# Kernel tuning notes

Hardware: AMD Instinct MI355X
Metric: run time of the kernel (lower is better)

## Reference

```python
import jax, jax.numpy as jnp
import numpy as np

SELECTOR = jnp.array([29, 49, 79])
N_FINAL = 6
N_EM_ITERS = 10
LOG_2PI = float(np.log(2.0 * np.pi))


def _logdet2(c):
    # log determinant of trailing 2x2 matrices
    return jnp.log(c[..., 0, 0] * c[..., 1, 1] - c[..., 0, 1] * c[..., 1, 0])


def _inv2(c):
    # analytic inverse of trailing 2x2 matrices
    det = c[..., 0, 0] * c[..., 1, 1] - c[..., 0, 1] * c[..., 1, 0]
    inv = jnp.stack([
        jnp.stack([c[..., 1, 1], -c[..., 0, 1]], axis=-1),
        jnp.stack([-c[..., 1, 0], c[..., 0, 0]], axis=-1),
    ], axis=-2)
    return inv / det[..., None, None]


def _initial_state(probas, trajectories):
    B, M = probas.shape
    tsel = trajectories[:, :, SELECTOR, :]                       # [B,M,3,2]
    dots = jnp.einsum('bmtd,bntd->btmn', tsel, tsel)             # [B,3,M,M]
    d1 = jnp.einsum('bmtd,bmtd->btm', tsel, tsel)                # [B,3,M]
    R = jnp.sqrt(d1[:, :, :, None] + d1[:, :, None, :] - 2.0 * dots)
    thr = jnp.quantile(R[:, -1].reshape(B, -1), 0.15, axis=-1)[:, None, None, None]
    adj = (R <= thr).astype(probas.dtype).prod(axis=1)           # [B,M,M]
    worked = jnp.ones((B, M), dtype=probas.dtype)
    bidx = jnp.arange(B)
    idxs = []
    for _ in range(N_FINAL):
        score = (adj * probas[:, None, :]).sum(axis=2) * worked  # [B,M]
        amax = jnp.argmax(score, axis=-1)                        # [B]
        worked = worked * (1.0 - adj[bidx, amax])
        idxs.append(amax)
    return jnp.stack(idxs, axis=1)                               # [B,6]


def _coefficients(cov6, trajectories, traj6, probas6):
    cov6_sel = cov6[:, :, SELECTOR]                              # [B,6,3,2,2]
    prec = _inv2(cov6_sel)                                       # [B,6,3,2,2]
    diff = traj6[:, :, SELECTOR][:, :, None] - trajectories[:, :, SELECTOR][:, None]  # [B,6,M,3,2]
    qform = jnp.einsum('bnmti,bntij,bnmtj->bnmt', diff, prec, diff)
    logdet = _logdet2(cov6_sel)[:, :, None, :]                   # [B,6,1,3]
    pM = jnp.exp((-LOG_2PI - 0.5 * logdet - 0.5 * qform).sum(axis=-1)) + 1e-8  # [B,6,M]
    num = pM * probas6[:, :, None]
    return num / (num.sum(axis=1, keepdims=True) + 1e-8)


def _forward(non_normalized_probas, trajectories, covariance_matrices):
    B = trajectories.shape[0]
    probas = jax.nn.softmax(non_normalized_probas, axis=-1)
    idx = jax.lax.stop_gradient(_initial_state(probas, trajectories))  # [B,6]
    b = jnp.arange(B)[:, None]
    traj6 = trajectories[b, idx]                                 # [B,6,T,2]
    probas6 = jax.nn.softmax(jnp.take_along_axis(non_normalized_probas, idx, axis=1), axis=-1)
    cov6 = covariance_matrices[b, idx]                           # [B,6,T,2,2]
    for _ in range(N_EM_ITERS):
        pM = jax.lax.stop_gradient(_coefficients(cov6, trajectories, traj6, probas6))
        P = probas[:, None, :] * pM                              # [B,6,M]
        probas6 = P.sum(axis=-1)                                 # [B,6]
        traj6 = jnp.einsum('bnm,bmtd->bntd', P, trajectories) / probas6[:, :, None, None]
        diff = traj6[:, :, None] - trajectories[:, None]         # [B,6,M,T,2]
        cov6 = (jnp.einsum('bnm,bmtij->bntij', P, covariance_matrices)
                + jnp.einsum('bnm,bnmti,bnmtj->bntij', P, diff, diff)) / probas6[:, :, None, None, None]
    return probas6, traj6, cov6


def setup_inputs() -> dict:
    key = jax.random.key(0)
    k1, k2, k3 = jax.random.split(key, 3)
    B, M, T = 256, 48, 80
    logits = jax.random.normal(k1, (B, M), dtype=jnp.float32)
    trajectories = jax.random.normal(k2, (B, M, T, 2), dtype=jnp.float32)
    A = 0.3 * jax.random.normal(k3, (B, M, T, 2, 2), dtype=jnp.float32)
    cov = A @ jnp.swapaxes(A, -1, -2) + 0.5 * jnp.eye(2, dtype=jnp.float32)
    return {'non_normalized_probas': logits, 'trajectories': trajectories,
            'covariance_matrices': cov}


def reference(non_normalized_probas, trajectories, covariance_matrices):
    return _forward(non_normalized_probas, trajectories, covariance_matrices)
```

## Files before the change

### kernel.cpp

```cpp
#include <hip/hip_runtime.h>
#include <math.h>

#define BATCH 256
#define M 48
#define T 80
#define NF 6
#define EMIT 10
#define MM (M*M)
#define NPT (MM/256)

#define LOG2PI 1.8378770664093453f

__global__ __launch_bounds__(256, 1)
void em_kernel(const float* __restrict__ g_logits,
               const float* __restrict__ g_traj,
               const float* __restrict__ g_cov,
               float* __restrict__ g_out)
{
    const int b = blockIdx.x;
    const int tid = threadIdx.x;
    const int lane = tid & 63;
    const int wv = tid >> 6;
    const int SEL[3] = {29, 49, 79};

    __shared__ __align__(16) float s_fxy[M*T*2];
    __shared__ __align__(16) float s_fc01[M*T*2];
    __shared__ float s_fc11[M*T];
    __shared__ float s_R2[MM];
    __shared__ float s_logits[M];
    __shared__ float s_probas[M];
    __shared__ float s_tsel[M*6];
    __shared__ float s_d1[M*3];
    __shared__ __align__(16) float s_csel[M*3*4];
    __shared__ __align__(16) float s_Pm[M*8];
    __shared__ float s_t6sel[NF*6];
    __shared__ float s_probas6[NF];
    __shared__ float s_prec[NF*3*3];
    __shared__ float s_ld[NF*3];
    __shared__ int   s_idx[NF];
    __shared__ unsigned s_hist[256];
    __shared__ unsigned s_wsum[4];
    __shared__ int s_seld;
    __shared__ int s_sele;

    const float* traj_b = g_traj + (size_t)b * (M*T*2);
    const float* cov_b  = g_cov  + (size_t)b * (M*T*4);

    if (tid < M) s_logits[tid] = g_logits[b*M + tid];
    {
        const float4* src = (const float4*)traj_b;
        float4* dst = (float4*)s_fxy;
        for (int i = tid; i < (M*T*2)/4; i += 256) dst[i] = src[i];
    }
    {
        const float4* src = (const float4*)cov_b;
        float2* dstc = (float2*)s_fc01;
        for (int i = tid; i < M*T; i += 256) {
            float4 c = src[i];
            dstc[i] = make_float2(c.x, c.y);
            s_fc11[i] = c.w;
        }
    }
    __syncthreads();

    if (wv == 0) {
        float lg = (lane < M) ? s_logits[lane] : -1e30f;
        float mx = lg;
        #pragma unroll
        for (int off = 32; off; off >>= 1) mx = fmaxf(mx, __shfl_xor(mx, off));
        float e = (lane < M) ? expf(lg - mx) : 0.f;
        float sum = e;
        #pragma unroll
        for (int off = 32; off; off >>= 1) sum += __shfl_xor(sum, off);
        if (lane < M) s_probas[lane] = e / sum;
    }
    if (tid >= 64 && tid < 64 + M*3) {
        int i = tid - 64;
        int m = i / 3, tt = i - (i/3)*3;
        float x = s_fxy[(m*T + SEL[tt])*2 + 0];
        float y = s_fxy[(m*T + SEL[tt])*2 + 1];
        s_tsel[m*6+tt*2+0] = x;
        s_tsel[m*6+tt*2+1] = y;
        s_d1[i] = x*x + y*y;
    }
    if (tid < M*3) {
        int m = tid / 3, tt = tid - (tid/3)*3;
        int src = m*T + SEL[tt];
        s_csel[tid*4+0] = s_fc01[src*2+0];
        s_csel[tid*4+1] = s_fc01[src*2+1];
        s_csel[tid*4+2] = s_fc11[src];
        s_csel[tid*4+3] = 0.f;
    }
    __syncthreads();

    for (int e = tid; e < MM; e += 256) {
        int m = e / M, n = e - (e/M)*M;
        float dot = s_tsel[m*6+4]*s_tsel[n*6+4] + s_tsel[m*6+5]*s_tsel[n*6+5];
        float v = s_d1[m*3+2] + s_d1[n*3+2] - 2.0f*dot;
        s_R2[e] = sqrtf(fmaxf(v, 0.0f));
    }
    __syncthreads();

    unsigned key[NPT];
    #pragma unroll
    for (int c = 0; c < NPT; ++c) key[c] = __float_as_uint(s_R2[tid + c*256]);

    int target = 345;
    unsigned prefix = 0u, pmask = 0u;
    for (int shift = 24; shift >= 0; shift -= 8) {
        s_hist[tid] = 0u;
        __syncthreads();
        #pragma unroll
        for (int c = 0; c < NPT; ++c) {
            if ((key[c] & pmask) == prefix)
                atomicAdd(&s_hist[(key[c] >> shift) & 255u], 1u);
        }
        __syncthreads();
        unsigned h = s_hist[tid];
        unsigned v = h;
        #pragma unroll
        for (int off = 1; off < 64; off <<= 1) {
            unsigned u = __shfl_up(v, off);
            if (lane >= off) v += u;
        }
        if (lane == 63) s_wsum[wv] = v;
        __syncthreads();
        unsigned pre = 0;
        for (int w = 0; w < wv; ++w) pre += s_wsum[w];
        unsigned exc = pre + v - h;
        if ((int)exc <= target && target < (int)(exc + h)) {
            s_seld = tid;
            s_sele = (int)exc;
        }
        __syncthreads();
        target -= s_sele;
        prefix |= ((unsigned)s_seld) << shift;
        pmask  |= (255u << shift);
    }
    const unsigned k1 = prefix;
    const float v1f = __uint_as_float(k1);

    {
        unsigned cnt = 0, mng = 0xFFFFFFFFu;
        #pragma unroll
        for (int c = 0; c < NPT; ++c) {
            if (key[c] <= k1) cnt++;
            else mng = (key[c] < mng) ? key[c] : mng;
        }
        #pragma unroll
        for (int off = 32; off > 0; off >>= 1) {
            cnt += __shfl_down(cnt, off);
            unsigned mo = __shfl_down(mng, off);
            mng = (mo < mng) ? mo : mng;
        }
        if (lane == 0) { s_hist[wv] = cnt; s_hist[4+wv] = mng; }
        __syncthreads();
        unsigned ctot = s_hist[0]+s_hist[1]+s_hist[2]+s_hist[3];
        unsigned mtot = s_hist[4];
        if (s_hist[5] < mtot) mtot = s_hist[5];
        if (s_hist[6] < mtot) mtot = s_hist[6];
        if (s_hist[7] < mtot) mtot = s_hist[7];
        unsigned k2 = (ctot >= 347u) ? k1 : mtot;
        const float v2f = __uint_as_float(k2);
        const float qi = 0.15f * 2303.0f;
        const float fr = qi - floorf(qi);
        float thr = v1f * (1.0f - fr) + v2f * fr;

        for (int e = tid; e < MM; e += 256) {
            int m = e / M, n = e - (e/M)*M;
            bool a = (s_R2[e] <= thr);
            float d0 = s_tsel[m*6+0]*s_tsel[n*6+0] + s_tsel[m*6+1]*s_tsel[n*6+1];
            float r0 = sqrtf(fmaxf(s_d1[m*3+0] + s_d1[n*3+0] - 2.0f*d0, 0.0f));
            float d1v = s_tsel[m*6+2]*s_tsel[n*6+2] + s_tsel[m*6+3]*s_tsel[n*6+3];
            float r1 = sqrtf(fmaxf(s_d1[m*3+1] + s_d1[n*3+1] - 2.0f*d1v, 0.0f));
            a = a && (r0 <= thr) && (r1 <= thr);
            s_R2[e] = a ? 1.0f : 0.0f;
        }
    }
    __syncthreads();
    #define s_adj s_R2

    if (wv == 0) {
        const int m = (lane < M) ? lane : (M-1);
        float adjcol[M];
        #pragma unroll
        for (int n = 0; n < M; ++n) adjcol[n] = s_adj[n*M + m];
        float base = 0.f;
        #pragma unroll
        for (int n = 0; n < M; ++n) base += adjcol[n] * s_probas[n];
        float worked = 1.f;
        #pragma unroll
        for (int k = 0; k < NF; ++k) {
            float sc = (lane < M) ? base * worked : -1.f;
            int bi = lane;
            #pragma unroll
            for (int off = 32; off; off >>= 1) {
                float so = __shfl_down(sc, off);
                int io = __shfl_down(bi, off);
                if (so > sc || (so == sc && io < bi)) { sc = so; bi = io; }
            }
            int amax = __shfl(bi, 0);
            if (lane == 0) s_idx[k] = amax;
            float arow = s_adj[amax*M + m];
            worked *= (1.f - arow);
        }
        if (lane < NF) {
            float mx = -1e30f;
            for (int j = 0; j < NF; ++j) mx = fmaxf(mx, s_logits[s_idx[j]]);
            float sum = 0.f;
            for (int j = 0; j < NF; ++j) sum += expf(s_logits[s_idx[j]] - mx);
            s_probas6[lane] = expf(s_logits[s_idx[lane]] - mx) / sum;
        }
        if (lane < NF*3) {
            int n = lane / 3, tt = lane - (lane/3)*3;
            int m0 = s_idx[n];
            s_t6sel[n*6+tt*2+0] = s_tsel[m0*6+tt*2+0];
            s_t6sel[n*6+tt*2+1] = s_tsel[m0*6+tt*2+1];
            float c00 = s_csel[(m0*3+tt)*4+0];
            float c01 = s_csel[(m0*3+tt)*4+1];
            float c11 = s_csel[(m0*3+tt)*4+2];
            float det = c00*c11 - c01*c01;
            s_prec[lane*3+0] =  c11 / det;
            s_prec[lane*3+1] = -c01 / det;
            s_prec[lane*3+2] =  c00 / det;
            s_ld[lane] = logf(det);
        }
    }
    __syncthreads();

    for (int it = 0; it < EMIT; ++it) {
        if (wv == 0) {
            const int m = (lane < M) ? lane : (M-1);
            float tm[6];
            #pragma unroll
            for (int j = 0; j < 6; ++j) tm[j] = s_tsel[m*6+j];
            float num[NF];
            float den = 1e-8f;
            #pragma unroll
            for (int n = 0; n < NF; ++n) {
                float q = 0.f, lds_ = 0.f;
                #pragma unroll
                for (int tt = 0; tt < 3; ++tt) {
                    float dx = s_t6sel[n*6+tt*2+0] - tm[tt*2+0];
                    float dy = s_t6sel[n*6+tt*2+1] - tm[tt*2+1];
                    float p00 = s_prec[(n*3+tt)*3+0];
                    float p01 = s_prec[(n*3+tt)*3+1];
                    float p11 = s_prec[(n*3+tt)*3+2];
                    q += p00*dx*dx + 2.0f*p01*dx*dy + p11*dy*dy;
                    lds_ += s_ld[n*3+tt];
                }
                float ex = -3.0f*LOG2PI - 0.5f*lds_ - 0.5f*q;
                num[n] = (expf(ex) + 1e-8f) * s_probas6[n];
                den += num[n];
            }
            float f = (lane < M) ? (s_probas[m] / den) : 0.f;
            float P[NF];
            #pragma unroll
            for (int n = 0; n < NF; ++n) P[n] = (lane < M) ? num[n]*f : 0.f;
            float s[NF];
            #pragma unroll
            for (int n = 0; n < NF; ++n) {
                float v = P[n];
                #pragma unroll
                for (int off = 32; off; off >>= 1) v += __shfl_down(v, off);
                s[n] = v;
            }
            if (lane < M) {
                *(float4*)&s_Pm[m*8]   = make_float4(P[0],P[1],P[2],P[3]);
                *(float2*)&s_Pm[m*8+4] = make_float2(P[4],P[5]);
            }
            if (lane == 0) {
                #pragma unroll
                for (int n = 0; n < NF; ++n) s_probas6[n] = s[n];
            }
        }
        __syncthreads();

        if (it < EMIT-1) {
            if (wv == 0 && lane < NF*3) {
                int n = lane / 3, tt = lane - (lane/3)*3;
                float S1x=0,S1y=0,Sxx=0,Sxy=0,Syy=0,C00=0,C01=0,C11=0;
                for (int m2 = 0; m2 < M; ++m2) {
                    float x = s_tsel[m2*6+tt*2+0];
                    float y = s_tsel[m2*6+tt*2+1];
                    float4 c = *(const float4*)&s_csel[(m2*3+tt)*4];
                    float p = s_Pm[m2*8+n];
                    S1x += p*x; S1y += p*y;
                    Sxx += p*x*x; Sxy += p*x*y; Syy += p*y*y;
                    C00 += p*c.x; C01 += p*c.y; C11 += p*c.z;
                }
                float p6 = s_probas6[n];
                float tx = S1x/p6, ty = S1y/p6;
                float c00 = (C00 + (Sxx - S1x*tx)) / p6;
                float c01 = (C01 + (Sxy - S1x*ty)) / p6;
                float c11 = (C11 + (Syy - S1y*ty)) / p6;
                float det = c00*c11 - c01*c01;
                s_prec[lane*3+0] =  c11 / det;
                s_prec[lane*3+1] = -c01 / det;
                s_prec[lane*3+2] =  c00 / det;
                s_ld[lane] = logf(det);
                s_t6sel[n*6+tt*2+0] = tx;
                s_t6sel[n*6+tt*2+1] = ty;
            }
            __syncthreads();
        }
    }

    float* out_p = g_out;
    float2* out_t = (float2*)(g_out + BATCH*NF);
    float4* out_c = (float4*)(g_out + BATCH*NF + BATCH*NF*T*2);
    if (tid < 240) {
        int np = tid / 80;
        int t  = tid - np*80;
        int n0 = np*2, n1 = n0 + 1;
        float S1x0=0,S1y0=0,Sxx0=0,Sxy0=0,Syy0=0,C000=0,C010=0,C110=0;
        float S1x1=0,S1y1=0,Sxx1=0,Sxy1=0,Syy1=0,C001=0,C011=0,C111=0;
        const float2* fxy = (const float2*)s_fxy;
        const float2* fc01 = (const float2*)s_fc01;
        const float2* pm2 = (const float2*)s_Pm;
        #pragma unroll 8
        for (int m2 = 0; m2 < M; ++m2) {
            float2 xy  = fxy[m2*T + t];
            float2 c01 = fc01[m2*T + t];
            float  c11 = s_fc11[m2*T + t];
            float2 pp  = pm2[m2*4 + np];
            float xx = xy.x*xy.x, xyv = xy.x*xy.y, yy = xy.y*xy.y;
            S1x0 += pp.x*xy.x;  S1y0 += pp.x*xy.y;
            Sxx0 += pp.x*xx;    Sxy0 += pp.x*xyv;  Syy0 += pp.x*yy;
            C000 += pp.x*c01.x; C010 += pp.x*c01.y; C110 += pp.x*c11;
            S1x1 += pp.y*xy.x;  S1y1 += pp.y*xy.y;
            Sxx1 += pp.y*xx;    Sxy1 += pp.y*xyv;  Syy1 += pp.y*yy;
            C001 += pp.y*c01.x; C011 += pp.y*c01.y; C111 += pp.y*c11;
        }
        float p60 = s_probas6[n0], p61 = s_probas6[n1];
        float tx0 = S1x0/p60, ty0 = S1y0/p60;
        float tx1 = S1x1/p61, ty1 = S1y1/p61;
        float c000 = (C000 + (Sxx0 - S1x0*tx0)) / p60;
        float c010 = (C010 + (Sxy0 - S1x0*ty0)) / p60;
        float c110 = (C110 + (Syy0 - S1y0*ty0)) / p60;
        float c001 = (C001 + (Sxx1 - S1x1*tx1)) / p61;
        float c011 = (C011 + (Sxy1 - S1x1*ty1)) / p61;
        float c111 = (C111 + (Syy1 - S1y1*ty1)) / p61;
        size_t base = (size_t)b*(NF*T);
        out_t[base + n0*T + t] = make_float2(tx0, ty0);
        out_t[base + n1*T + t] = make_float2(tx1, ty1);
        out_c[base + n0*T + t] = make_float4(c000, c010, c010, c110);
        out_c[base + n1*T + t] = make_float4(c001, c011, c011, c111);
    }
    if (tid < NF) out_p[b*NF + tid] = s_probas6[tid];
}

extern "C" void kernel_launch(void* const* d_in, const int* in_sizes, int n_in,
                              void* d_out, int out_size, void* d_ws, size_t ws_size,
                              hipStream_t stream) {
    const float* logits = (const float*)d_in[0];
    const float* traj   = (const float*)d_in[1];
    const float* cov    = (const float*)d_in[2];
    float* out = (float*)d_out;
    em_kernel<<<dim3(BATCH), dim3(256), 0, stream>>>(logits, traj, cov, out);
}
```

Before: 122.3 us.

## Rewrite EM kernel as single-wavefront block with async LDS loads and histogram quantile

Shrinks each block from 256 threads to one 64-lane wavefront, which removes all __syncthreads barriers. Bulk trajectory and covariance data are copied with global_load_lds DMA, split into stages so the copies overlap the distance, quantile and greedy-selection work. The 4-pass radix select becomes a value-scaled histogram plus a candidate rank within the chosen bin. The EM M-step is spread across 54 lanes, and the final per-timestep reduction now runs 64 lanes over all six components. Risks include less parallelism per block for the final reduction, correctness of the bin-candidate cap of 192, and reliance on a raw s_waitcnt value plus the DMA writes being visible to LDS reads.

```diff
diff --git a/kernel.cpp b/kernel.cpp
--- a/kernel.cpp
+++ b/kernel.cpp
@@ -7,26 +7,27 @@
 #define NF 6
 #define EMIT 10
 #define MM (M*M)
-#define NPT (MM/256)
-
+#define KPL (MM/64)
+#define NBIN 256
+#define CAP 192
 #define LOG2PI 1.8378770664093453f
 
-__global__ __launch_bounds__(256, 1)
+typedef unsigned int u32;
+typedef unsigned long long u64;
+
+__global__ __launch_bounds__(64, 1)
 void em_kernel(const float* __restrict__ g_logits,
                const float* __restrict__ g_traj,
                const float* __restrict__ g_cov,
                float* __restrict__ g_out)
 {
     const int b = blockIdx.x;
-    const int tid = threadIdx.x;
-    const int lane = tid & 63;
-    const int wv = tid >> 6;
+    const int lane = threadIdx.x;
     const int SEL[3] = {29, 49, 79};
 
-    __shared__ __align__(16) float s_fxy[M*T*2];
-    __shared__ __align__(16) float s_fc01[M*T*2];
-    __shared__ float s_fc11[M*T];
-    __shared__ float s_R2[MM];
+    __shared__ __align__(16) float s_txy[M*T*2];
+    __shared__ __align__(16) float s_cv4[M*T*4];
+    __shared__ float s_adj[MM];
     __shared__ float s_logits[M];
     __shared__ float s_probas[M];
     __shared__ float s_tsel[M*6];
@@ -38,160 +39,182 @@
     __shared__ float s_prec[NF*3*3];
     __shared__ float s_ld[NF*3];
     __shared__ int   s_idx[NF];
-    __shared__ unsigned s_hist[256];
-    __shared__ unsigned s_wsum[4];
-    __shared__ int s_seld;
-    __shared__ int s_sele;
-
-    const float* traj_b = g_traj + (size_t)b * (M*T*2);
-    const float* cov_b  = g_cov  + (size_t)b * (M*T*4);
-
-    if (tid < M) s_logits[tid] = g_logits[b*M + tid];
+    __shared__ u32   s_hist[NBIN];
+    __shared__ u32   s_cand[CAP];
+    __shared__ u32   s_cnt;
+    __shared__ float s_v[2];
+
+    const float* traj_b = g_traj + (size_t)b*(M*T*2);
+    const float* cov_b  = g_cov  + (size_t)b*(M*T*4);
+
+    float myLogit = -1e30f;
+    if (lane < M) myLogit = g_logits[b*M + lane];
+    float selx[3], sely[3], cc0[3], cc1[3], cc2[3];
+    #pragma unroll
+    for (int r = 0; r < 3; ++r) {
+        int i = lane + r*64;
+        if (i < M*3) {
+            int m = i/3, tt = i - (i/3)*3;
+            float2 xy = ((const float2*)traj_b)[m*T + SEL[tt]];
+            float4 cv = ((const float4*)cov_b)[m*T + SEL[tt]];
+            selx[r]=xy.x; sely[r]=xy.y; cc0[r]=cv.x; cc1[r]=cv.y; cc2[r]=cv.w;
+        }
+    }
+    if (lane < M) s_logits[lane] = myLogit;
+    #pragma unroll
+    for (int r = 0; r < 3; ++r) {
+        int i = lane + r*64;
+        if (i < M*3) {
+            int m = i/3, tt = i - (i/3)*3;
+            s_tsel[m*6+tt*2+0] = selx[r];
+            s_tsel[m*6+tt*2+1] = sely[r];
+            s_d1[i] = selx[r]*selx[r] + sely[r]*sely[r];
+            s_csel[i*4+0]=cc0[r]; s_csel[i*4+1]=cc1[r]; s_csel[i*4+2]=cc2[r]; s_csel[i*4+3]=0.f;
+        }
+    }
+
+    __builtin_amdgcn_sched_barrier(0);
     {
-        const float4* src = (const float4*)traj_b;
-        float4* dst = (float4*)s_fxy;
-        for (int i = tid; i < (M*T*2)/4; i += 256) dst[i] = src[i];
-    }
-    {
-        const float4* src = (const float4*)cov_b;
-        float2* dstc = (float2*)s_fc01;
-        for (int i = tid; i < M*T; i += 256) {
-            float4 c = src[i];
-            dstc[i] = make_float2(c.x, c.y);
-            s_fc11[i] = c.w;
-        }
-    }
-    __syncthreads();
-
-    if (wv == 0) {
-        float lg = (lane < M) ? s_logits[lane] : -1e30f;
-        float mx = lg;
-        #pragma unroll
-        for (int off = 32; off; off >>= 1) mx = fmaxf(mx, __shfl_xor(mx, off));
-        float e = (lane < M) ? expf(lg - mx) : 0.f;
-        float sum = e;
-        #pragma unroll
-        for (int off = 32; off; off >>= 1) sum += __shfl_xor(sum, off);
-        if (lane < M) s_probas[lane] = e / sum;
-    }
-    if (tid >= 64 && tid < 64 + M*3) {
-        int i = tid - 64;
-        int m = i / 3, tt = i - (i/3)*3;
-        float x = s_fxy[(m*T + SEL[tt])*2 + 0];
-        float y = s_fxy[(m*T + SEL[tt])*2 + 1];
-        s_tsel[m*6+tt*2+0] = x;
-        s_tsel[m*6+tt*2+1] = y;
-        s_d1[i] = x*x + y*y;
-    }
-    if (tid < M*3) {
-        int m = tid / 3, tt = tid - (tid/3)*3;
-        int src = m*T + SEL[tt];
-        s_csel[tid*4+0] = s_fc01[src*2+0];
-        s_csel[tid*4+1] = s_fc01[src*2+1];
-        s_csel[tid*4+2] = s_fc11[src];
-        s_csel[tid*4+3] = 0.f;
-    }
-    __syncthreads();
-
-    for (int e = tid; e < MM; e += 256) {
-        int m = e / M, n = e - (e/M)*M;
+        const char* gt = (const char*)traj_b + lane*16;
+        #pragma unroll
+        for (int k = 0; k < 30; ++k)
+            __builtin_amdgcn_global_load_lds(
+                (const __attribute__((address_space(1))) u32*)(gt + k*1024),
+                (__attribute__((address_space(3))) u32*)((char*)s_txy + k*1024), 16, 0, 0);
+    }
+    __builtin_amdgcn_sched_barrier(0);
+
+    float mx = myLogit;
+    #pragma unroll
+    for (int off = 32; off; off >>= 1) mx = fmaxf(mx, __shfl_xor(mx, off));
+    float pe = (lane < M) ? expf(myLogit - mx) : 0.f;
+    float psum = pe;
+    #pragma unroll
+    for (int off = 32; off; off >>= 1) psum += __shfl_xor(psum, off);
+    const float proba = pe / psum;
+    if (lane < M) s_probas[lane] = proba;
+
+    float key[KPL];
+    #pragma unroll
+    for (int c = 0; c < KPL; ++c) {
+        int e = lane + c*64;
+        int m = e/M, n = e - (e/M)*M;
         float dot = s_tsel[m*6+4]*s_tsel[n*6+4] + s_tsel[m*6+5]*s_tsel[n*6+5];
         float v = s_d1[m*3+2] + s_d1[n*3+2] - 2.0f*dot;
-        s_R2[e] = sqrtf(fmaxf(v, 0.0f));
-    }
-    __syncthreads();
-
-    unsigned key[NPT];
-    #pragma unroll
-    for (int c = 0; c < NPT; ++c) key[c] = __float_as_uint(s_R2[tid + c*256]);
-
-    int target = 345;
-    unsigned prefix = 0u, pmask = 0u;
-    for (int shift = 24; shift >= 0; shift -= 8) {
-        s_hist[tid] = 0u;
-        __syncthreads();
-        #pragma unroll
-        for (int c = 0; c < NPT; ++c) {
-            if ((key[c] & pmask) == prefix)
-                atomicAdd(&s_hist[(key[c] >> shift) & 255u], 1u);
-        }
-        __syncthreads();
-        unsigned h = s_hist[tid];
-        unsigned v = h;
-        #pragma unroll
-        for (int off = 1; off < 64; off <<= 1) {
-            unsigned u = __shfl_up(v, off);
-            if (lane >= off) v += u;
-        }
-        if (lane == 63) s_wsum[wv] = v;
-        __syncthreads();
-        unsigned pre = 0;
-        for (int w = 0; w < wv; ++w) pre += s_wsum[w];
-        unsigned exc = pre + v - h;
-        if ((int)exc <= target && target < (int)(exc + h)) {
-            s_seld = tid;
-            s_sele = (int)exc;
-        }
-        __syncthreads();
-        target -= s_sele;
-        prefix |= ((unsigned)s_seld) << shift;
-        pmask  |= (255u << shift);
-    }
-    const unsigned k1 = prefix;
-    const float v1f = __uint_as_float(k1);
-
+        key[c] = sqrtf(fmaxf(v, 0.0f));
+    }
+    float kmax = 0.f;
+    #pragma unroll
+    for (int c = 0; c < KPL; ++c) kmax = fmaxf(kmax, key[c]);
+    #pragma unroll
+    for (int off = 32; off; off >>= 1) kmax = fmaxf(kmax, __shfl_xor(kmax, off));
+    const float scale = 256.0f / kmax;
+
+    s_hist[lane]=0; s_hist[lane+64]=0; s_hist[lane+128]=0; s_hist[lane+192]=0;
+    #pragma unroll
+    for (int c = 0; c < KPL; ++c) {
+        int bin = (int)(key[c]*scale); bin = bin > 255 ? 255 : bin;
+        atomicAdd(&s_hist[bin], 1u);
+    }
+    uint4 hv = ((const uint4*)s_hist)[lane];
+    u32 s4 = hv.x + hv.y + hv.z + hv.w;
+    u32 cum = s4;
+    #pragma unroll
+    for (int off = 1; off < 64; off <<= 1) {
+        u32 u = __shfl_up(cum, off);
+        if (lane >= off) cum += u;
+    }
+
+    #pragma unroll 1
+    for (int ri = 0; ri < 2; ++ri) {
+        const u32 target = 345u + (u32)ri;
+        u64 bmask = __ballot(cum > target);
+        int g = __builtin_ctzll(bmask);
+        int binIdx = 0; u32 binStart = 0;
+        if (lane == g) {
+            u32 exc = cum - s4;
+            int bi2 = lane*4;
+            if (exc + hv.x > target)      { binIdx = bi2;   binStart = exc; }
+            else { exc += hv.x;
+                if (exc + hv.y > target)  { binIdx = bi2+1; binStart = exc; }
+                else { exc += hv.y;
+                    if (exc + hv.z > target) { binIdx = bi2+2; binStart = exc; }
+                    else { exc += hv.z;       binIdx = bi2+3; binStart = exc; } } }
+        }
+        binIdx   = __shfl(binIdx, g);
+        binStart = (u32)__shfl((int)binStart, g);
+        if (lane == 0) s_cnt = 0;
+        #pragma unroll
+        for (int c = 0; c < KPL; ++c) {
+            int bin = (int)(key[c]*scale); bin = bin > 255 ? 255 : bin;
+            if (bin == binIdx) {
+                u32 p = atomicAdd(&s_cnt, 1u);
+                if (p < CAP) s_cand[p] = __float_as_uint(key[c]);
+            }
+        }
+        u32 cnt = s_cnt; if (cnt > CAP) cnt = CAP;
+        u32 own0=0xFFFFFFFFu, own1=0xFFFFFFFFu, own2=0xFFFFFFFFu;
+        if ((u32)lane      < cnt) own0 = s_cand[lane];
+        if ((u32)lane+64u  < cnt) own1 = s_cand[lane+64];
+        if ((u32)lane+128u < cnt) own2 = s_cand[lane+128];
+        u32 cl0=0,ce0=0, cl1=0,ce1=0, cl2=0,ce2=0;
+        for (u32 i = 0; i < cnt; ++i) {
+            u32 v = s_cand[i];
+            cl0 += (v < own0); ce0 += (v == own0);
+            cl1 += (v < own1); ce1 += (v == own1);
+            cl2 += (v < own2); ce2 += (v == own2);
+        }
+        if ((u32)lane      < cnt && binStart+cl0 <= target && target < binStart+cl0+ce0) s_v[ri] = __uint_as_float(own0);
+        if ((u32)lane+64u  < cnt && binStart+cl1 <= target && target < binStart+cl1+ce1) s_v[ri] = __uint_as_float(own1);
+        if ((u32)lane+128u < cnt && binStart+cl2 <= target && target < binStart+cl2+ce2) s_v[ri] = __uint_as_float(own2);
+    }
+    const float qi = 0.15f * 2303.0f;
+    const float fr = qi - floorf(qi);
+    const float thr = s_v[0]*(1.0f - fr) + s_v[1]*fr;
+
+    __builtin_amdgcn_sched_barrier(0);
     {
-        unsigned cnt = 0, mng = 0xFFFFFFFFu;
-        #pragma unroll
-        for (int c = 0; c < NPT; ++c) {
-            if (key[c] <= k1) cnt++;
-            else mng = (key[c] < mng) ? key[c] : mng;
-        }
-        #pragma unroll
-        for (int off = 32; off > 0; off >>= 1) {
-            cnt += __shfl_down(cnt, off);
-            unsigned mo = __shfl_down(mng, off);
-            mng = (mo < mng) ? mo : mng;
-        }
-        if (lane == 0) { s_hist[wv] = cnt; s_hist[4+wv] = mng; }
-        __syncthreads();
-        unsigned ctot = s_hist[0]+s_hist[1]+s_hist[2]+s_hist[3];
-        unsigned mtot = s_hist[4];
-        if (s_hist[5] < mtot) mtot = s_hist[5];
-        if (s_hist[6] < mtot) mtot = s_hist[6];
-        if (s_hist[7] < mtot) mtot = s_hist[7];
-        unsigned k2 = (ctot >= 347u) ? k1 : mtot;
-        const float v2f = __uint_as_float(k2);
-        const float qi = 0.15f * 2303.0f;
-        const float fr = qi - floorf(qi);
-        float thr = v1f * (1.0f - fr) + v2f * fr;
-
-        for (int e = tid; e < MM; e += 256) {
-            int m = e / M, n = e - (e/M)*M;
-            bool a = (s_R2[e] <= thr);
-            float d0 = s_tsel[m*6+0]*s_tsel[n*6+0] + s_tsel[m*6+1]*s_tsel[n*6+1];
-            float r0 = sqrtf(fmaxf(s_d1[m*3+0] + s_d1[n*3+0] - 2.0f*d0, 0.0f));
-            float d1v = s_tsel[m*6+2]*s_tsel[n*6+2] + s_tsel[m*6+3]*s_tsel[n*6+3];
-            float r1 = sqrtf(fmaxf(s_d1[m*3+1] + s_d1[n*3+1] - 2.0f*d1v, 0.0f));
-            a = a && (r0 <= thr) && (r1 <= thr);
-            s_R2[e] = a ? 1.0f : 0.0f;
-        }
-    }
-    __syncthreads();
-    #define s_adj s_R2
-
-    if (wv == 0) {
-        const int m = (lane < M) ? lane : (M-1);
-        float adjcol[M];
-        #pragma unroll
-        for (int n = 0; n < M; ++n) adjcol[n] = s_adj[n*M + m];
+        const char* gc = (const char*)cov_b + lane*16;
+        #pragma unroll
+        for (int k = 0; k < 30; ++k)
+            __builtin_amdgcn_global_load_lds(
+                (const __attribute__((address_space(1))) u32*)(gc + k*1024),
+                (__attribute__((address_space(3))) u32*)((char*)s_cv4 + k*1024), 16, 0, 0);
+    }
+    __builtin_amdgcn_sched_barrier(0);
+
+    #pragma unroll
+    for (int c = 0; c < KPL; ++c) {
+        int e = lane + c*64;
+        int m = e/M, n = e - (e/M)*M;
+        float d0 = s_tsel[m*6+0]*s_tsel[n*6+0] + s_tsel[m*6+1]*s_tsel[n*6+1];
+        float r0 = sqrtf(fmaxf(s_d1[m*3+0] + s_d1[n*3+0] - 2.0f*d0, 0.0f));
+        float d1v = s_tsel[m*6+2]*s_tsel[n*6+2] + s_tsel[m*6+3]*s_tsel[n*6+3];
+        float r1 = sqrtf(fmaxf(s_d1[m*3+1] + s_d1[n*3+1] - 2.0f*d1v, 0.0f));
+        bool a = (key[c] <= thr) && (r0 <= thr) && (r1 <= thr);
+        s_adj[e] = a ? 1.0f : 0.0f;
+    }
+
+    __builtin_amdgcn_sched_barrier(0);
+    {
+        const char* gc = (const char*)cov_b + lane*16;
+        #pragma unroll
+        for (int k = 30; k < 60; ++k)
+            __builtin_amdgcn_global_load_lds(
+                (const __attribute__((address_space(1))) u32*)(gc + k*1024),
+                (__attribute__((address_space(3))) u32*)((char*)s_cv4 + k*1024), 16, 0, 0);
+    }
+    __builtin_amdgcn_sched_barrier(0);
+
+    const int m = (lane < M) ? lane : (M-1);
+    {
         float base = 0.f;
         #pragma unroll
-        for (int n = 0; n < M; ++n) base += adjcol[n] * s_probas[n];
+        for (int n = 0; n < M; ++n) base += s_adj[n*M+m] * s_probas[n];
         float worked = 1.f;
-        #pragma unroll
+        #pragma unroll 1
         for (int k = 0; k < NF; ++k) {
-            float sc = (lane < M) ? base * worked : -1.f;
+            float sc = (lane < M) ? base*worked : -1.f;
             int bi = lane;
             #pragma unroll
             for (int off = 32; off; off >>= 1) {
@@ -201,153 +224,134 @@
             }
             int amax = __shfl(bi, 0);
             if (lane == 0) s_idx[k] = amax;
-            float arow = s_adj[amax*M + m];
-            worked *= (1.f - arow);
-        }
-        if (lane < NF) {
-            float mx = -1e30f;
-            for (int j = 0; j < NF; ++j) mx = fmaxf(mx, s_logits[s_idx[j]]);
-            float sum = 0.f;
-            for (int j = 0; j < NF; ++j) sum += expf(s_logits[s_idx[j]] - mx);
-            s_probas6[lane] = expf(s_logits[s_idx[lane]] - mx) / sum;
-        }
-        if (lane < NF*3) {
-            int n = lane / 3, tt = lane - (lane/3)*3;
-            int m0 = s_idx[n];
-            s_t6sel[n*6+tt*2+0] = s_tsel[m0*6+tt*2+0];
-            s_t6sel[n*6+tt*2+1] = s_tsel[m0*6+tt*2+1];
-            float c00 = s_csel[(m0*3+tt)*4+0];
-            float c01 = s_csel[(m0*3+tt)*4+1];
-            float c11 = s_csel[(m0*3+tt)*4+2];
-            float det = c00*c11 - c01*c01;
-            s_prec[lane*3+0] =  c11 / det;
-            s_prec[lane*3+1] = -c01 / det;
-            s_prec[lane*3+2] =  c00 / det;
-            s_ld[lane] = logf(det);
-        }
-    }
-    __syncthreads();
-
+            worked *= (1.f - s_adj[amax*M+m]);
+        }
+    }
+
+    if (lane < NF) {
+        float mx6 = -1e30f;
+        for (int j = 0; j < NF; ++j) mx6 = fmaxf(mx6, s_logits[s_idx[j]]);
+        float sum6 = 0.f;
+        for (int j = 0; j < NF; ++j) sum6 += expf(s_logits[s_idx[j]] - mx6);
+        s_probas6[lane] = expf(s_logits[s_idx[lane]] - mx6) / sum6;
+    }
+    if (lane < NF*3) {
+        int n = lane/3, tt = lane - (lane/3)*3;
+        int m0 = s_idx[n];
+        s_t6sel[n*6+tt*2+0] = s_tsel[m0*6+tt*2+0];
+        s_t6sel[n*6+tt*2+1] = s_tsel[m0*6+tt*2+1];
+        float c00 = s_csel[(m0*3+tt)*4+0];
+        float c01 = s_csel[(m0*3+tt)*4+1];
+        float c11 = s_csel[(m0*3+tt)*4+2];
+        float det = c00*c11 - c01*c01;
+        s_prec[lane*3+0] =  c11/det;
+        s_prec[lane*3+1] = -c01/det;
+        s_prec[lane*3+2] =  c00/det;
+        s_ld[lane] = logf(det);
+    }
+
+    float tm0=s_tsel[m*6+0], tm1=s_tsel[m*6+1], tm2=s_tsel[m*6+2],
+          tm3=s_tsel[m*6+3], tm4=s_tsel[m*6+4], tm5=s_tsel[m*6+5];
+    const int item  = lane/3;
+    const int chunk = lane - item*3;
+    const int mn    = item/3;
+    const int mtt   = item - (item/3)*3;
+
+    #pragma unroll 1
     for (int it = 0; it < EMIT; ++it) {
-        if (wv == 0) {
-            const int m = (lane < M) ? lane : (M-1);
-            float tm[6];
-            #pragma unroll
-            for (int j = 0; j < 6; ++j) tm[j] = s_tsel[m*6+j];
-            float num[NF];
-            float den = 1e-8f;
-            #pragma unroll
-            for (int n = 0; n < NF; ++n) {
-                float q = 0.f, lds_ = 0.f;
-                #pragma unroll
-                for (int tt = 0; tt < 3; ++tt) {
-                    float dx = s_t6sel[n*6+tt*2+0] - tm[tt*2+0];
-                    float dy = s_t6sel[n*6+tt*2+1] - tm[tt*2+1];
-                    float p00 = s_prec[(n*3+tt)*3+0];
-                    float p01 = s_prec[(n*3+tt)*3+1];
-                    float p11 = s_prec[(n*3+tt)*3+2];
-                    q += p00*dx*dx + 2.0f*p01*dx*dy + p11*dy*dy;
-                    lds_ += s_ld[n*3+tt];
-                }
-                float ex = -3.0f*LOG2PI - 0.5f*lds_ - 0.5f*q;
-                num[n] = (expf(ex) + 1e-8f) * s_probas6[n];
-                den += num[n];
+        float num[NF]; float den = 1e-8f;
+        #pragma unroll
+        for (int n = 0; n < NF; ++n) {
+            float lsum = s_ld[n*3+0] + s_ld[n*3+1] + s_ld[n*3+2];
+            float dx0 = s_t6sel[n*6+0]-tm0, dy0 = s_t6sel[n*6+1]-tm1;
+            float dx1 = s_t6sel[n*6+2]-tm2, dy1 = s_t6sel[n*6+3]-tm3;
+            float dx2 = s_t6sel[n*6+4]-tm4, dy2 = s_t6sel[n*6+5]-tm5;
+            float q = s_prec[(n*3+0)*3+0]*dx0*dx0 + 2.f*s_prec[(n*3+0)*3+1]*dx0*dy0 + s_prec[(n*3+0)*3+2]*dy0*dy0
+                    + s_prec[(n*3+1)*3+0]*dx1*dx1 + 2.f*s_prec[(n*3+1)*3+1]*dx1*dy1 + s_prec[(n*3+1)*3+2]*dy1*dy1
+                    + s_prec[(n*3+2)*3+0]*dx2*dx2 + 2.f*s_prec[(n*3+2)*3+1]*dx2*dy2 + s_prec[(n*3+2)*3+2]*dy2*dy2;
+            num[n] = (expf(-3.f*LOG2PI - 0.5f*lsum - 0.5f*q) + 1e-8f) * s_probas6[n];
+            den += num[n];
+        }
+        float f = proba / den;
+        if (lane < M) {
+            *(float4*)&s_Pm[m*8]   = make_float4(num[0]*f, num[1]*f, num[2]*f, num[3]*f);
+            *(float2*)&s_Pm[m*8+4] = make_float2(num[4]*f, num[5]*f);
+        }
+        if (it == EMIT-1) break;
+
+        if (lane < 54) {
+            float SP=0,S1x=0,S1y=0,Sxx=0,Sxy=0,Syy=0,Cs0=0,Cs1=0,Cs2=0;
+            int mbase = chunk*16;
+            #pragma unroll 4
+            for (int k = 0; k < 16; ++k) {
+                int mm = mbase + k;
+                float p = s_Pm[mm*8+mn];
+                float x = s_tsel[mm*6+mtt*2+0];
+                float y = s_tsel[mm*6+mtt*2+1];
+                float4 c4 = *(const float4*)&s_csel[(mm*3+mtt)*4];
+                SP += p; S1x += p*x; S1y += p*y;
+                Sxx += p*x*x; Sxy += p*x*y; Syy += p*y*y;
+                Cs0 += p*c4.x; Cs1 += p*c4.y; Cs2 += p*c4.z;
             }
-            float f = (lane < M) ? (s_probas[m] / den) : 0.f;
-            float P[NF];
-            #pragma unroll
-            for (int n = 0; n < NF; ++n) P[n] = (lane < M) ? num[n]*f : 0.f;
-            float s[NF];
-            #pragma unroll
-            for (int n = 0; n < NF; ++n) {
-                float v = P[n];
-                #pragma unroll
-                for (int off = 32; off; off >>= 1) v += __shfl_down(v, off);
-                s[n] = v;
+            #define CMB(v) { float a1_=__shfl_down(v,1), a2_=__shfl_down(v,2); v += a1_ + a2_; }
+            CMB(SP) CMB(S1x) CMB(S1y) CMB(Sxx) CMB(Sxy) CMB(Syy) CMB(Cs0) CMB(Cs1) CMB(Cs2)
+            if (chunk == 0) {
+                float p6 = SP;
+                if (mtt == 0) s_probas6[mn] = SP;
+                float tx = S1x/p6, ty = S1y/p6;
+                float c00 = (Cs0 + (Sxx - S1x*tx)) / p6;
+                float c01 = (Cs1 + (Sxy - S1x*ty)) / p6;
+                float c11 = (Cs2 + (Syy - S1y*ty)) / p6;
+                float det = c00*c11 - c01*c01;
+                s_prec[item*3+0] =  c11/det;
+                s_prec[item*3+1] = -c01/det;
+                s_prec[item*3+2] =  c00/det;
+                s_ld[item] = logf(det);
+                s_t6sel[mn*6+mtt*2+0] = tx;
+                s_t6sel[mn*6+mtt*2+1] = ty;
             }
-            if (lane < M) {
-                *(float4*)&s_Pm[m*8]   = make_float4(P[0],P[1],P[2],P[3]);
-                *(float2*)&s_Pm[m*8+4] = make_float2(P[4],P[5]);
-            }
-            if (lane == 0) {
-                #pragma unroll
-                for (int n = 0; n < NF; ++n) s_probas6[n] = s[n];
-            }
-        }
-        __syncthreads();
-
-        if (it < EMIT-1) {
-            if (wv == 0 && lane < NF*3) {
-                int n = lane / 3, tt = lane - (lane/3)*3;
-                float S1x=0,S1y=0,Sxx=0,Sxy=0,Syy=0,C00=0,C01=0,C11=0;
-                for (int m2 = 0; m2 < M; ++m2) {
-                    float x = s_tsel[m2*6+tt*2+0];
-                    float y = s_tsel[m2*6+tt*2+1];
-                    float4 c = *(const float4*)&s_csel[(m2*3+tt)*4];
-                    float p = s_Pm[m2*8+n];
-                    S1x += p*x; S1y += p*y;
-                    Sxx += p*x*x; Sxy += p*x*y; Syy += p*y*y;
-                    C00 += p*c.x; C01 += p*c.y; C11 += p*c.z;
-                }
-                float p6 = s_probas6[n];
-                float tx = S1x/p6, ty = S1y/p6;
-                float c00 = (C00 + (Sxx - S1x*tx)) / p6;
-                float c01 = (C01 + (Sxy - S1x*ty)) / p6;
-                float c11 = (C11 + (Syy - S1y*ty)) / p6;
-                float det = c00*c11 - c01*c01;
-                s_prec[lane*3+0] =  c11 / det;
-                s_prec[lane*3+1] = -c01 / det;
-                s_prec[lane*3+2] =  c00 / det;
-                s_ld[lane] = logf(det);
-                s_t6sel[n*6+tt*2+0] = tx;
-                s_t6sel[n*6+tt*2+1] = ty;
-            }
-            __syncthreads();
-        }
-    }
-
-    float* out_p = g_out;
+        }
+    }
+
+    __builtin_amdgcn_s_waitcnt(0x0F70);
+    float*  out_p = g_out;
     float2* out_t = (float2*)(g_out + BATCH*NF);
     float4* out_c = (float4*)(g_out + BATCH*NF + BATCH*NF*T*2);
-    if (tid < 240) {
-        int np = tid / 80;
-        int t  = tid - np*80;
-        int n0 = np*2, n1 = n0 + 1;
-        float S1x0=0,S1y0=0,Sxx0=0,Sxy0=0,Syy0=0,C000=0,C010=0,C110=0;
-        float S1x1=0,S1y1=0,Sxx1=0,Sxy1=0,Syy1=0,C001=0,C011=0,C111=0;
-        const float2* fxy = (const float2*)s_fxy;
-        const float2* fc01 = (const float2*)s_fc01;
-        const float2* pm2 = (const float2*)s_Pm;
-        #pragma unroll 8
-        for (int m2 = 0; m2 < M; ++m2) {
-            float2 xy  = fxy[m2*T + t];
-            float2 c01 = fc01[m2*T + t];
-            float  c11 = s_fc11[m2*T + t];
-            float2 pp  = pm2[m2*4 + np];
+    #pragma unroll 1
+    for (int t = lane; t < T; t += 64) {
+        float SP[NF]={0,0,0,0,0,0}, S1x[NF]={0,0,0,0,0,0}, S1y[NF]={0,0,0,0,0,0};
+        float Sxx[NF]={0,0,0,0,0,0}, Sxy[NF]={0,0,0,0,0,0}, Syy[NF]={0,0,0,0,0,0};
+        float C00[NF]={0,0,0,0,0,0}, C01[NF]={0,0,0,0,0,0}, C11[NF]={0,0,0,0,0,0};
+        #pragma unroll 2
+        for (int mm = 0; mm < M; ++mm) {
+            float2 xy = ((const float2*)s_txy)[mm*T + t];
+            float4 c4 = ((const float4*)s_cv4)[mm*T + t];
+            float4 Pa = *(const float4*)&s_Pm[mm*8];
+            float2 Pb = *(const float2*)&s_Pm[mm*8+4];
             float xx = xy.x*xy.x, xyv = xy.x*xy.y, yy = xy.y*xy.y;
-            S1x0 += pp.x*xy.x;  S1y0 += pp.x*xy.y;
-            Sxx0 += pp.x*xx;    Sxy0 += pp.x*xyv;  Syy0 += pp.x*yy;
-            C000 += pp.x*c01.x; C010 += pp.x*c01.y; C110 += pp.x*c11;
-            S1x1 += pp.y*xy.x;  S1y1 += pp.y*xy.y;
-            Sxx1 += pp.y*xx;    Sxy1 += pp.y*xyv;  Syy1 += pp.y*yy;
-            C001 += pp.y*c01.x; C011 += pp.y*c01.y; C111 += pp.y*c11;
-        }
-        float p60 = s_probas6[n0], p61 = s_probas6[n1];
-        float tx0 = S1x0/p60, ty0 = S1y0/p60;
-        float tx1 = S1x1/p61, ty1 = S1y1/p61;
-        float c000 = (C000 + (Sxx0 - S1x0*tx0)) / p60;
-        float c010 = (C010 + (Sxy0 - S1x0*ty0)) / p60;
-        float c110 = (C110 + (Syy0 - S1y0*ty0)) / p60;
-        float c001 = (C001 + (Sxx1 - S1x1*tx1)) / p61;
-        float c011 = (C011 + (Sxy1 - S1x1*ty1)) / p61;
-        float c111 = (C111 + (Syy1 - S1y1*ty1)) / p61;
-        size_t base = (size_t)b*(NF*T);
-        out_t[base + n0*T + t] = make_float2(tx0, ty0);
-        out_t[base + n1*T + t] = make_float2(tx1, ty1);
-        out_c[base + n0*T + t] = make_float4(c000, c010, c010, c110);
-        out_c[base + n1*T + t] = make_float4(c001, c011, c011, c111);
-    }
-    if (tid < NF) out_p[b*NF + tid] = s_probas6[tid];
+            #define UPD(p, n) { SP[n]+=(p); S1x[n]+=(p)*xy.x; S1y[n]+=(p)*xy.y; \
+                Sxx[n]+=(p)*xx; Sxy[n]+=(p)*xyv; Syy[n]+=(p)*yy; \
+                C00[n]+=(p)*c4.x; C01[n]+=(p)*c4.y; C11[n]+=(p)*c4.w; }
+            UPD(Pa.x,0) UPD(Pa.y,1) UPD(Pa.z,2) UPD(Pa.w,3) UPD(Pb.x,4) UPD(Pb.y,5)
+            #undef UPD
+        }
+        #pragma unroll
+        for (int n = 0; n < NF; ++n) {
+            float p6 = SP[n];
+            float tx = S1x[n]/p6, ty = S1y[n]/p6;
+            float c00 = (C00[n] + (Sxx[n] - S1x[n]*tx)) / p6;
+            float c01 = (C01[n] + (Sxy[n] - S1x[n]*ty)) / p6;
+            float c11 = (C11[n] + (Syy[n] - S1y[n]*ty)) / p6;
+            size_t o = (size_t)(b*NF + n)*T + t;
+            out_t[o] = make_float2(tx, ty);
+            out_c[o] = make_float4(c00, c01, c01, c11);
+        }
+    }
+    if (lane < NF) {
+        float sp = 0.f;
+        for (int mm = 0; mm < M; ++mm) sp += s_Pm[mm*8+lane];
+        out_p[b*NF + lane] = sp;
+    }
 }
 
 extern "C" void kernel_launch(void* const* d_in, const int* in_sizes, int n_in,
@@ -357,5 +361,5 @@
     const float* traj   = (const float*)d_in[1];
     const float* cov    = (const float*)d_in[2];
     float* out = (float*)d_out;
-    em_kernel<<<dim3(BATCH), dim3(256), 0, stream>>>(logits, traj, cov, out);
+    em_kernel<<<dim3(BATCH), dim3(64), 0, stream>>>(logits, traj, cov, out);
 }
```

Measured after the change: 128.1 us. 4.8% more time.
